# Optimization experiments

Hardware: AMD Instinct MI355X
Metric: run time of the kernel (lower is better)

## Reference

```python
import jax, jax.numpy as jnp
import numpy as np

N_NODES = 50000
N_EDGES = 800000
D_IN = 256
D_OUT = 256
N_REL = 8


def setup_inputs() -> dict:
    key = jax.random.key(0)
    k_x, k_ei, k_et, k_w = jax.random.split(key, 4)
    x = jax.random.normal(k_x, (N_NODES, D_IN), dtype=jnp.float32)
    edge_index = jax.random.randint(k_ei, (2, N_EDGES), 0, N_NODES, dtype=jnp.int32)
    edge_type = jax.random.randint(k_et, (N_EDGES,), 0, N_REL, dtype=jnp.int32)
    # xavier_uniform-style init for per-relation weights [R, I, O]
    limit = float(np.sqrt(6.0 / (D_IN + D_OUT)))
    weight = jax.random.uniform(k_w, (N_REL, D_IN, D_OUT), dtype=jnp.float32,
                                minval=-limit, maxval=limit)
    bias = jnp.zeros((D_OUT,), dtype=jnp.float32)
    return {"x": x, "edge_index": edge_index, "edge_type": edge_type,
            "weight": weight, "bias": bias}


def reference(x, edge_index, edge_type, weight, bias):
    # RGCN (block / per-relation weights):
    #   out[row] += x[col] @ weight[edge_type]
    # Vectorized: transform every node under every relation once (dense GEMM),
    # then gather the right (relation, col) slice per edge and scatter-add to row.
    num_nodes = x.shape[0]
    row, col = edge_index[0], edge_index[1]
    xt = jnp.einsum('ni,rio->rno', x, weight)          # [R, N, O]
    messages = xt[edge_type, col]                       # [E, O]
    out = jax.ops.segment_sum(messages, row, num_segments=num_nodes)  # [N, O]
    return jax.nn.relu(out + bias)
```

## Files before the change

kernel.cpp:

```cpp
#include <hip/hip_runtime.h>
#include <hip/hip_bf16.h>
#include <stdint.h>

typedef __attribute__((ext_vector_type(8))) short short8;
typedef __attribute__((ext_vector_type(4))) float f32x4;

#define D 256

static __device__ __forceinline__ float b2f(unsigned short u) {
  union { unsigned u; float f; } c; c.u = ((unsigned)u) << 16; return c.f;
}
static __device__ __forceinline__ unsigned short f2b(float f) {
  union { float f; unsigned u; } c; c.f = f;
  unsigned r = (c.u + 0x7FFFu + ((c.u >> 16) & 1u)) >> 16;
  return (unsigned short)r;
}

static __device__ __forceinline__ void gload16(const void* g, void* l) {
  __builtin_amdgcn_global_load_lds(
      (const __attribute__((address_space(1))) unsigned int*)g,
      (__attribute__((address_space(3))) unsigned int*)l, 16, 0, 0);
}

__global__ void k_cvt_x(const float* __restrict__ x, unsigned short* __restrict__ xb,
                        long n_elems, long pad_elems) {
  long i4 = (long)blockIdx.x * 256 + threadIdx.x;
  if (i4 * 4 >= pad_elems) return;
  ushort4 o;
  if (i4 * 4 < n_elems) {
    float4 v = ((const float4*)x)[i4];
    o.x = f2b(v.x); o.y = f2b(v.y); o.z = f2b(v.z); o.w = f2b(v.w);
  } else {
    o.x = 0; o.y = 0; o.z = 0; o.w = 0;
  }
  ((ushort4*)xb)[i4] = o;
}

__global__ void k_cvt_w(const float* __restrict__ w, unsigned short* __restrict__ wt,
                        int total) {
  int t = blockIdx.x * 256 + threadIdx.x;
  if (t >= total) return;
  int i = t & 255;
  int orow = t >> 8;
  int r = orow >> 8, o = orow & 255;
  wt[t] = f2b(w[((size_t)(r * 256 + i)) * 256 + o]);
}

__global__ __launch_bounds__(256) void k_gemm(const unsigned short* __restrict__ A,
                                              const unsigned short* __restrict__ B,
                                              unsigned short* __restrict__ C,
                                              int ldc, int nty) {
  __shared__ __align__(16) char lA[64 * 512];
  __shared__ __align__(16) char lB[128 * 128];
  const int t = threadIdx.x;
  const int lane = t & 63;
  const int wave = t >> 6;
  const int l15 = lane & 15, lhi = lane >> 4;
  const size_t tm = (size_t)blockIdx.x * 64;

#pragma unroll
  for (int it = 0; it < 8; ++it) {
    int s = it * 256 + t;
    int row = s >> 5, c = s & 31;
    gload16(A + (tm + row) * 256 + ((c ^ (row & 7)) * 8),
            lA + (it * 256 + wave * 64) * 16);
  }

  for (int y = 0; y < nty; ++y) {
    const int tn = y * 128;
    f32x4 acc[4][2];
#pragma unroll
    for (int a = 0; a < 4; ++a)
#pragma unroll
      for (int b = 0; b < 2; ++b)
#pragma unroll
        for (int e = 0; e < 4; ++e) acc[a][b][e] = 0.f;

    for (int kt = 0; kt < 256; kt += 64) {
      __syncthreads();
#pragma unroll
      for (int it = 0; it < 4; ++it) {
        int s = it * 256 + t;
        int row = s >> 3, c = s & 7;
        gload16(B + (tn + row) * 256 + kt + ((c ^ (row & 7)) * 8),
                lB + (it * 256 + wave * 64) * 16);
      }
      __syncthreads();

      short8 af[4][2], bfv[2][2];
      const int ktc = kt >> 3;
#pragma unroll
      for (int mi = 0; mi < 4; ++mi) {
#pragma unroll
        for (int kk = 0; kk < 2; ++kk) {
          int R = mi * 16 + l15;
          int c = ktc + kk * 4 + lhi;
          af[mi][kk] = *(const short8*)(lA + R * 512 + ((c ^ (R & 7)) * 16));
        }
      }
#pragma unroll
      for (int ni = 0; ni < 2; ++ni) {
#pragma unroll
        for (int kk = 0; kk < 2; ++kk) {
          int R2 = wave * 32 + ni * 16 + l15;
          int c2 = kk * 4 + lhi;
          bfv[ni][kk] = *(const short8*)(lB + R2 * 128 + ((c2 ^ (R2 & 7)) * 16));
        }
      }
#pragma unroll
      for (int mi = 0; mi < 4; ++mi) {
#pragma unroll
        for (int ni = 0; ni < 2; ++ni) {
          acc[mi][ni] = __builtin_amdgcn_mfma_f32_16x16x32_bf16(af[mi][0], bfv[ni][0], acc[mi][ni], 0, 0, 0);
          acc[mi][ni] = __builtin_amdgcn_mfma_f32_16x16x32_bf16(af[mi][1], bfv[ni][1], acc[mi][ni], 0, 0, 0);
        }
      }
    }
#pragma unroll
    for (int mi = 0; mi < 4; ++mi) {
#pragma unroll
      for (int j = 0; j < 4; ++j) {
        size_t row = tm + mi * 16 + lhi * 4 + j;
        unsigned pk = (unsigned)f2b(acc[mi][0][j]) | ((unsigned)f2b(acc[mi][1][j]) << 16);
        *(unsigned*)(C + row * (size_t)ldc + tn + wave * 32 + l15 * 2) = pk;
      }
    }
  }
}

__global__ void k_zero(int* p, int n) {
  int i = blockIdx.x * 256 + threadIdx.x;
  if (i < n) p[i] = 0;
}
__global__ void k_deg(const int* __restrict__ ei, int* deg, int E) {
  int e = blockIdx.x * 256 + threadIdx.x;
  if (e < E) atomicAdd(&deg[ei[e]], 1);
}
__global__ void k_scan1(const int* __restrict__ deg, int* bsum, int n) {
  __shared__ int sm[256];
  int t = threadIdx.x, idx = blockIdx.x * 256 + t;
  sm[t] = idx < n ? deg[idx] : 0;
  __syncthreads();
  for (int off = 128; off; off >>= 1) {
    if (t < off) sm[t] += sm[t + off];
    __syncthreads();
  }
  if (t == 0) bsum[blockIdx.x] = sm[0];
}
__global__ void k_scan2(const int* __restrict__ bsum, int* boff, int* rowptr,
                        int nsc, int Nn) {
  __shared__ int sm[256];
  int t = threadIdx.x;
  int v = t < nsc ? bsum[t] : 0;
  sm[t] = v;
  __syncthreads();
  for (int off = 1; off < 256; off <<= 1) {
    int x = t >= off ? sm[t - off] : 0;
    __syncthreads();
    sm[t] += x;
    __syncthreads();
  }
  if (t < nsc) boff[t] = sm[t] - v;
  if (t == nsc - 1) rowptr[Nn] = sm[t];
}
__global__ void k_scan3(const int* __restrict__ deg, const int* __restrict__ boff,
                        int* rowptr, int* cursor, int n) {
  __shared__ int sm[256];
  int t = threadIdx.x, idx = blockIdx.x * 256 + t;
  int v = idx < n ? deg[idx] : 0;
  sm[t] = v;
  __syncthreads();
  for (int off = 1; off < 256; off <<= 1) {
    int x = t >= off ? sm[t - off] : 0;
    __syncthreads();
    sm[t] += x;
    __syncthreads();
  }
  if (idx < n) {
    int e = boff[blockIdx.x] + sm[t] - v;
    rowptr[idx] = e;
    cursor[idx] = e;
  }
}
__global__ void k_bin(const int* __restrict__ ei, const int* __restrict__ et,
                      int* cursor, unsigned* ect, int E) {
  int e = blockIdx.x * 256 + threadIdx.x;
  if (e >= E) return;
  int r = ei[e], c = ei[E + e], ty = et[e];
  int pos = atomicAdd(&cursor[r], 1);
  ect[pos] = (unsigned)c | ((unsigned)ty << 20);
}

__global__ __launch_bounds__(256) void k_gather(const unsigned* __restrict__ ect,
                                                const int* __restrict__ rowptr,
                                                const unsigned short* __restrict__ xt,
                                                const float* __restrict__ bias,
                                                float* __restrict__ out, int n, int ldxt) {
  __shared__ float sm[4][256];
  int lane = threadIdx.x & 63;
  int wid = threadIdx.x >> 6;
  int row = blockIdx.x * 4 + wid;
  if (row >= n) return;
  int s = rowptr[row], e = rowptr[row + 1];
  float a0 = 0.f, a1 = 0.f, a2 = 0.f, a3 = 0.f;
  unsigned myct = (s + lane < e) ? ect[s + lane] : 0u;
  int cnt = e - s;
  if (cnt > 64) cnt = 64;
  for (int i = 0; i < cnt; ++i) {
    unsigned ct = __shfl(myct, i);
    size_t base = (size_t)(ct & 0xFFFFFu) * ldxt + ((ct >> 20) << 8) + (lane << 2);
    ushort4 v = *(const ushort4*)(xt + base);
    a0 += b2f(v.x); a1 += b2f(v.y); a2 += b2f(v.z); a3 += b2f(v.w);
  }
  for (int i = s + 64; i < e; ++i) {
    unsigned ct = ect[i];
    size_t base = (size_t)(ct & 0xFFFFFu) * ldxt + ((ct >> 20) << 8) + (lane << 2);
    ushort4 v = *(const ushort4*)(xt + base);
    a0 += b2f(v.x); a1 += b2f(v.y); a2 += b2f(v.z); a3 += b2f(v.w);
  }
  int p0 = lane * 4;
  float av[4] = {a0, a1, a2, a3};
#pragma unroll
  for (int q = 0; q < 4; ++q) {
    int p8 = p0 + q;
    int o = (p8 & 224) | ((p8 & 1) << 4) | ((p8 & 31) >> 1);
    sm[wid][o] = av[q];
  }
  float4 v = *(const float4*)&sm[wid][lane * 4];
  float4 bb = ((const float4*)bias)[lane];
  float4 o;
  o.x = fmaxf(v.x + bb.x, 0.f);
  o.y = fmaxf(v.y + bb.y, 0.f);
  o.z = fmaxf(v.z + bb.z, 0.f);
  o.w = fmaxf(v.w + bb.w, 0.f);
  ((float4*)out)[(size_t)row * 64 + lane] = o;
}

extern "C" void kernel_launch(void* const* d_in, const int* in_sizes, int n_in,
                              void* d_out, int out_size, void* d_ws, size_t ws_size,
                              hipStream_t stream) {
  const float* x = (const float*)d_in[0];
  const int* ei = (const int*)d_in[1];
  const int* et = (const int*)d_in[2];
  const float* w = (const float*)d_in[3];
  const float* bias = (const float*)d_in[4];
  float* out = (float*)d_out;

  const int Nn = in_sizes[0] / D;
  const int E = in_sizes[2];
  const int R = in_sizes[3] / (D * D);
  const int Mpad = ((Nn + 63) / 64) * 64;
  const int NC = R * D;

  char* p = (char*)d_ws;
  auto alloc = [&](size_t bytes) -> char* {
    char* q = p;
    p += (bytes + 255) & ~(size_t)255;
    return q;
  };
  unsigned short* xt = (unsigned short*)alloc((size_t)Mpad * NC * 2);
  unsigned short* xb = (unsigned short*)alloc((size_t)Mpad * D * 2);
  unsigned short* wt = (unsigned short*)alloc((size_t)NC * D * 2);
  int* rowptr = (int*)alloc((size_t)(Nn + 1) * 4);
  int* cursor = (int*)alloc((size_t)Nn * 4);
  int* deg = (int*)alloc((size_t)Nn * 4);
  int* bsum = (int*)alloc(1024);
  int* boff = (int*)alloc(1024);
  unsigned* ect = (unsigned*)alloc((size_t)E * 4);

  const int nsc = (Nn + 255) / 256;

  hipLaunchKernelGGL(k_zero, dim3(nsc), dim3(256), 0, stream, deg, Nn);
  hipLaunchKernelGGL(k_deg, dim3((E + 255) / 256), dim3(256), 0, stream, ei, deg, E);
  hipLaunchKernelGGL(k_scan1, dim3(nsc), dim3(256), 0, stream, deg, bsum, Nn);
  hipLaunchKernelGGL(k_scan2, dim3(1), dim3(256), 0, stream, bsum, boff, rowptr, nsc, Nn);
  hipLaunchKernelGGL(k_scan3, dim3(nsc), dim3(256), 0, stream, deg, boff, rowptr, cursor, Nn);
  hipLaunchKernelGGL(k_bin, dim3((E + 255) / 256), dim3(256), 0, stream, ei, et, cursor, ect, E);

  hipLaunchKernelGGL(k_cvt_x, dim3(Mpad / 4), dim3(256), 0, stream, x, xb,
                     (long)Nn * D, (long)Mpad * D);
  hipLaunchKernelGGL(k_cvt_w, dim3((NC * D + 255) / 256), dim3(256), 0, stream, w, wt, NC * D);
  hipLaunchKernelGGL(k_gemm, dim3(Mpad / 64), dim3(256), 0, stream, xb, wt, xt, NC, NC / 128);

  hipLaunchKernelGGL(k_gather, dim3((Nn + 3) / 4), dim3(256), 0, stream, ect, rowptr,
                     xt, bias, out, Nn, NC);
}
```

Before: 391.3 us.

## Restructure GEMM: 256-wide N tiles, 2D grid split, register-prefetched B loads

The GEMM kernel now splits the relation/output columns across a second grid dimension, with each block handling two 256-wide column tiles. The output tile per block grows from 64x128 to 64x256. Direct global-to-LDS loads are replaced by register-staged loads, and the next B tile is prefetched into registers while the current one is consumed, overlapping memory latency with MFMA work. This gives more blocks for parallelism and more reuse of the A fragments, at the cost of more VGPRs (accumulators plus prefetch buffers), which may reduce occupancy. Each block also reloads its A tile, so A is read once per blockIdx.y.

```diff
diff --git a/kernel.cpp b/kernel.cpp
--- a/kernel.cpp
+++ b/kernel.cpp
@@ -6,6 +6,7 @@
 typedef __attribute__((ext_vector_type(4))) float f32x4;
 
 #define D 256
+#define NYB 2
 
 static __device__ __forceinline__ float b2f(unsigned short u) {
   union { unsigned u; float f; } c; c.u = ((unsigned)u) << 16; return c.f;
@@ -14,12 +15,6 @@
   union { float f; unsigned u; } c; c.f = f;
   unsigned r = (c.u + 0x7FFFu + ((c.u >> 16) & 1u)) >> 16;
   return (unsigned short)r;
-}
-
-static __device__ __forceinline__ void gload16(const void* g, void* l) {
-  __builtin_amdgcn_global_load_lds(
-      (const __attribute__((address_space(1))) unsigned int*)g,
-      (__attribute__((address_space(3))) unsigned int*)l, 16, 0, 0);
 }
 
 __global__ void k_cvt_x(const float* __restrict__ x, unsigned short* __restrict__ xb,
@@ -49,81 +44,103 @@
 __global__ __launch_bounds__(256) void k_gemm(const unsigned short* __restrict__ A,
                                               const unsigned short* __restrict__ B,
                                               unsigned short* __restrict__ C,
-                                              int ldc, int nty) {
+                                              int ldc) {
   __shared__ __align__(16) char lA[64 * 512];
-  __shared__ __align__(16) char lB[128 * 128];
+  __shared__ __align__(16) char lB[256 * 128];
   const int t = threadIdx.x;
   const int lane = t & 63;
   const int wave = t >> 6;
   const int l15 = lane & 15, lhi = lane >> 4;
   const size_t tm = (size_t)blockIdx.x * 64;
-
+  const int y0 = blockIdx.y * NYB;
+
+  uint4 ta[8];
 #pragma unroll
   for (int it = 0; it < 8; ++it) {
     int s = it * 256 + t;
     int row = s >> 5, c = s & 31;
-    gload16(A + (tm + row) * 256 + ((c ^ (row & 7)) * 8),
-            lA + (it * 256 + wave * 64) * 16);
-  }
-
-  for (int y = 0; y < nty; ++y) {
-    const int tn = y * 128;
-    f32x4 acc[4][2];
-#pragma unroll
-    for (int a = 0; a < 4; ++a)
-#pragma unroll
-      for (int b = 0; b < 2; ++b)
-#pragma unroll
-        for (int e = 0; e < 4; ++e) acc[a][b][e] = 0.f;
-
-    for (int kt = 0; kt < 256; kt += 64) {
-      __syncthreads();
-#pragma unroll
-      for (int it = 0; it < 4; ++it) {
+    ta[it] = *(const uint4*)(A + (tm + row) * 256 + c * 8);
+  }
+  uint4 rb[8];
+#pragma unroll
+  for (int it = 0; it < 8; ++it) {
+    int s = it * 256 + t;
+    int row = s >> 3, c = s & 7;
+    rb[it] = *(const uint4*)(B + ((size_t)(y0 * 256 + row)) * 256 + c * 8);
+  }
+#pragma unroll
+  for (int it = 0; it < 8; ++it) {
+    int s = it * 256 + t;
+    int row = s >> 5, c = s & 31;
+    *(uint4*)(lA + row * 512 + ((c ^ (row & 7)) * 16)) = ta[it];
+  }
+
+  f32x4 acc[4][4];
+  for (int q = 0; q < NYB * 4; ++q) {
+    const int kt = (q & 3) * 64;
+    if (kt == 0) {
+#pragma unroll
+      for (int a = 0; a < 4; ++a)
+#pragma unroll
+        for (int b = 0; b < 4; ++b)
+#pragma unroll
+          for (int e = 0; e < 4; ++e) acc[a][b][e] = 0.f;
+    }
+    __syncthreads();
+#pragma unroll
+    for (int it = 0; it < 8; ++it) {
+      int s = it * 256 + t;
+      int row = s >> 3, c = s & 7;
+      *(uint4*)(lB + row * 128 + ((c ^ (row & 7)) * 16)) = rb[it];
+    }
+    if (q + 1 < NYB * 4) {
+      int kt2 = ((q + 1) & 3) * 64;
+      int y2 = y0 + ((q + 1) >> 2);
+#pragma unroll
+      for (int it = 0; it < 8; ++it) {
         int s = it * 256 + t;
         int row = s >> 3, c = s & 7;
-        gload16(B + (tn + row) * 256 + kt + ((c ^ (row & 7)) * 8),
-                lB + (it * 256 + wave * 64) * 16);
+        rb[it] = *(const uint4*)(B + ((size_t)(y2 * 256 + row)) * 256 + kt2 + c * 8);
       }
-      __syncthreads();
-
-      short8 af[4][2], bfv[2][2];
-      const int ktc = kt >> 3;
+    }
+    __syncthreads();
+
+    const int ktc = kt >> 3;
+    short8 af[4][2];
+#pragma unroll
+    for (int mi = 0; mi < 4; ++mi)
+#pragma unroll
+      for (int kk = 0; kk < 2; ++kk) {
+        int R = mi * 16 + l15;
+        int c = ktc + kk * 4 + lhi;
+        af[mi][kk] = *(const short8*)(lA + R * 512 + ((c ^ (R & 7)) * 16));
+      }
+#pragma unroll
+    for (int ni = 0; ni < 4; ++ni) {
+      int R2 = wave * 64 + ni * 16 + l15;
+      short8 b0 = *(const short8*)(lB + R2 * 128 + (((lhi) ^ (R2 & 7)) * 16));
+      short8 b1 = *(const short8*)(lB + R2 * 128 + (((4 + lhi) ^ (R2 & 7)) * 16));
 #pragma unroll
       for (int mi = 0; mi < 4; ++mi) {
-#pragma unroll
-        for (int kk = 0; kk < 2; ++kk) {
-          int R = mi * 16 + l15;
-          int c = ktc + kk * 4 + lhi;
-          af[mi][kk] = *(const short8*)(lA + R * 512 + ((c ^ (R & 7)) * 16));
+        acc[mi][ni] = __builtin_amdgcn_mfma_f32_16x16x32_bf16(af[mi][0], b0, acc[mi][ni], 0, 0, 0);
+        acc[mi][ni] = __builtin_amdgcn_mfma_f32_16x16x32_bf16(af[mi][1], b1, acc[mi][ni], 0, 0, 0);
+      }
+    }
+
+    if ((q & 3) == 3) {
+      const int tn = (y0 + (q >> 2)) * 256;
+#pragma unroll
+      for (int mi = 0; mi < 4; ++mi)
+#pragma unroll
+        for (int j = 0; j < 4; ++j) {
+          size_t row = tm + mi * 16 + lhi * 4 + j;
+#pragma unroll
+          for (int bl = 0; bl < 2; ++bl) {
+            unsigned pk = (unsigned)f2b(acc[mi][bl * 2][j]) |
+                          ((unsigned)f2b(acc[mi][bl * 2 + 1][j]) << 16);
+            *(unsigned*)(C + row * (size_t)ldc + tn + (wave * 2 + bl) * 32 + l15 * 2) = pk;
+          }
         }
-      }
-#pragma unroll
-      for (int ni = 0; ni < 2; ++ni) {
-#pragma unroll
-        for (int kk = 0; kk < 2; ++kk) {
-          int R2 = wave * 32 + ni * 16 + l15;
-          int c2 = kk * 4 + lhi;
-          bfv[ni][kk] = *(const short8*)(lB + R2 * 128 + ((c2 ^ (R2 & 7)) * 16));
-        }
-      }
-#pragma unroll
-      for (int mi = 0; mi < 4; ++mi) {
-#pragma unroll
-        for (int ni = 0; ni < 2; ++ni) {
-          acc[mi][ni] = __builtin_amdgcn_mfma_f32_16x16x32_bf16(af[mi][0], bfv[ni][0], acc[mi][ni], 0, 0, 0);
-          acc[mi][ni] = __builtin_amdgcn_mfma_f32_16x16x32_bf16(af[mi][1], bfv[ni][1], acc[mi][ni], 0, 0, 0);
-        }
-      }
-    }
-#pragma unroll
-    for (int mi = 0; mi < 4; ++mi) {
-#pragma unroll
-      for (int j = 0; j < 4; ++j) {
-        size_t row = tm + mi * 16 + lhi * 4 + j;
-        unsigned pk = (unsigned)f2b(acc[mi][0][j]) | ((unsigned)f2b(acc[mi][1][j]) << 16);
-        *(unsigned*)(C + row * (size_t)ldc + tn + wave * 32 + l15 * 2) = pk;
-      }
     }
   }
 }
@@ -280,7 +297,8 @@
   hipLaunchKernelGGL(k_cvt_x, dim3(Mpad / 4), dim3(256), 0, stream, x, xb,
                      (long)Nn * D, (long)Mpad * D);
   hipLaunchKernelGGL(k_cvt_w, dim3((NC * D + 255) / 256), dim3(256), 0, stream, w, wt, NC * D);
-  hipLaunchKernelGGL(k_gemm, dim3(Mpad / 64), dim3(256), 0, stream, xb, wt, xt, NC, NC / 128);
+  hipLaunchKernelGGL(k_gemm, dim3(Mpad / 64, NC / (256 * NYB)), dim3(256), 0, stream,
+                     xb, wt, xt, NC);
 
   hipLaunchKernelGGL(k_gather, dim3((Nn + 3) / 4), dim3(256), 0, stream, ect, rowptr,
                      xt, bias, out, Nn, NC);
```

Measured after the change: 535.9 us. 37.0% more time.
